# Kernel optimization log

Measured on AMD Instinct MI355X. Metric: run time of the kernel, lower is better.

## Reference

```python
import jax, jax.numpy as jnp
import numpy as np

EPS = 0.05  # blend weight of K_Rectify smoothing


def k_rectify(x_nbc, distance, idx, eps=EPS):
    """Distance-weighted neighbor smoothing.
    x_nbc: (N, B, C); distance, idx: (B, N, K). Returns (N, B, C)."""
    x_bnc = jnp.transpose(x_nbc, (1, 0, 2))                       # (B,N,C)
    B = x_bnc.shape[0]
    neigh = x_bnc[jnp.arange(B)[:, None, None], idx]              # (B,N,K,C) gather
    w = jax.nn.softmax(-distance, axis=-1)                        # closer -> larger weight
    smoothed = jnp.einsum('bnk,bnkc->bnc', w, neigh)              # (B,N,C)
    y = (1.0 - eps) * x_bnc + eps * smoothed
    return jnp.transpose(y, (1, 0, 2))


def monarch_linear(x, w1, w2, bias):
    """Monarch block-diagonal butterfly multiply on the last dim.
    w1: (k,q,p), w2: (l,s,r) with k*p == n, l*r == k*q."""
    shp = x.shape
    k, q, p = w1.shape
    l, s, r = w2.shape
    xb = x.reshape(-1, k, p)
    o1 = jnp.einsum('kqp,bkp->bkq', w1, xb)                       # (B*, k, q)
    o1 = o1.reshape(-1, r, l).transpose(0, 2, 1)                  # 'b (r l) -> b l r'
    o2 = jnp.einsum('lsr,blr->bls', w2, o1)                       # (B*, l, s)
    out = o2.transpose(0, 2, 1).reshape(-1, s * l) + bias         # 'b l s -> b (s l)'
    return out.reshape(*shp[:-1], s * l)


def setup_inputs() -> dict:
    key = jax.random.key(0)
    B, N, C, K, nblocks = 8, 8192, 256, 8, 8
    blk = C // nblocks
    ks = jax.random.split(key, 6)
    x = jax.random.normal(ks[0], (B, N, C), dtype=jnp.float32)
    distance = jax.random.uniform(ks[1], (B, N, K), dtype=jnp.float32)
    idx = jax.random.randint(ks[2], (B, N, K), 0, N)
    rf = jax.random.normal(ks[3], (B, N, C), dtype=jnp.float32)
    scale = 1.0 / np.sqrt(blk)
    w1 = jax.random.normal(ks[4], (nblocks, blk, blk), dtype=jnp.float32) * scale
    w2 = jax.random.normal(ks[5], (nblocks, blk, blk), dtype=jnp.float32) * scale
    bias = jnp.zeros((C,), dtype=jnp.float32)
    return {"x": x, "distance": distance, "idx": idx, "rf": rf,
            "w1": w1, "w2": w2, "bias": bias}


def reference(x, distance, idx, rf, w1, w2, bias):
    # _prepare_in: (B,N,C) -> (N,B,C)
    xs = jnp.transpose(x, (1, 0, 2))
    s1 = k_rectify(xs, distance, idx)            # smooth_in
    t = monarch_linear(s1, w1, w2, bias)         # Monarch block-diag matmul
    s2 = k_rectify(t, distance, idx)             # smooth_out
    return jnp.transpose(s2, (1, 0, 2)) + rf     # _out_transform residual
```

## Files before the change

kernel.cpp:

```cpp
#include <hip/hip_runtime.h>

#define NPTS 8192
#define CH   256
#define KNB  8
#define NROWS 65536
#define ROWS_PER_BLK 16
#define ROWS_PER_IT  4
#define FT_STRIDE 36

typedef unsigned short ushort_t;

__device__ __forceinline__ ushort_t f32_to_bf16(float f) {
    unsigned int b = __float_as_uint(f);
    b += 0x7FFFu + ((b >> 16) & 1u);
    return (ushort_t)(b >> 16);
}
__device__ __forceinline__ float bf16_to_f32(ushort_t u) {
    return __uint_as_float(((unsigned int)u) << 16);
}
__device__ __forceinline__ unsigned int pack_bf16(float lo, float hi) {
    return (unsigned int)f32_to_bf16(lo) | ((unsigned int)f32_to_bf16(hi) << 16);
}

__global__ __launch_bounds__(256) void pm_conv(
    const float4* __restrict__ x, uint4* __restrict__ xb)
{
    const size_t i = (size_t)blockIdx.x * 256 + threadIdx.x;
    const float4 a = x[2 * i];
    const float4 c = x[2 * i + 1];
    uint4 o;
    o.x = pack_bf16(a.x, a.y);
    o.y = pack_bf16(a.z, a.w);
    o.z = pack_bf16(c.x, c.y);
    o.w = pack_bf16(c.z, c.w);
    xb[i] = o;
}

__global__ __launch_bounds__(256) void pm_stage1(
    const ushort_t* __restrict__ xb, const float* __restrict__ dist,
    const int* __restrict__ idx, const float* __restrict__ w1,
    const float* __restrict__ w2, const float* __restrict__ bias,
    ushort_t* __restrict__ t)
{
    const int c = threadIdx.x;

    __shared__ float s1[ROWS_PER_IT][CH];
    __shared__ float fT[ROWS_PER_IT][8 * FT_STRIDE];

    float4 w1r[8], w2r[8];
    {
        const float4* w1p = (const float4*)(w1 + c * 32);
        const float4* w2p = (const float4*)(w2 + ((c & 7) * 32 + (c >> 3)) * 32);
#pragma unroll
        for (int i = 0; i < 8; ++i) { w1r[i] = w1p[i]; w2r[i] = w2p[i]; }
    }
    const float bb = bias[c];
    const int l2   = c & 7;
    const int kb   = c >> 5;
    const int ftw  = l2 * FT_STRIDE + (c >> 3);

    const int rr   = __builtin_amdgcn_readfirstlane(threadIdx.x >> 6);
    const int lane = threadIdx.x & 63;

    const int row_base = blockIdx.x * ROWS_PER_BLK;
    const int b = row_base >> 13;
    const ushort4* x4 = (const ushort4*)(xb + (size_t)b * NPTS * CH);

    for (int it = 0; it < ROWS_PER_BLK / ROWS_PER_IT; ++it) {
        const int row  = row_base + it * ROWS_PER_IT + rr;
        const int rloc = row & (NPTS - 1);

        float d[KNB]; int nb[KNB];
#pragma unroll
        for (int k = 0; k < KNB; ++k) {
            d[k]  = dist[(size_t)row * KNB + k];
            nb[k] = idx[(size_t)row * KNB + k];
        }

        const ushort4 c0 = x4[(size_t)rloc * 64 + lane];
        ushort4 g[KNB];
#pragma unroll
        for (int k = 0; k < KNB; ++k) g[k] = x4[(size_t)nb[k] * 64 + lane];

        float mn = d[0];
#pragma unroll
        for (int k = 1; k < KNB; ++k) mn = fminf(mn, d[k]);
        float e[KNB]; float sum = 0.f;
#pragma unroll
        for (int k = 0; k < KNB; ++k) { e[k] = __expf(mn - d[k]); sum += e[k]; }
        const float inv = 0.05f / sum;

        float4 acc;
        acc.x = 0.95f * bf16_to_f32(c0.x);
        acc.y = 0.95f * bf16_to_f32(c0.y);
        acc.z = 0.95f * bf16_to_f32(c0.z);
        acc.w = 0.95f * bf16_to_f32(c0.w);
#pragma unroll
        for (int k = 0; k < KNB; ++k) {
            const float w = e[k] * inv;
            acc.x += w * bf16_to_f32(g[k].x);
            acc.y += w * bf16_to_f32(g[k].y);
            acc.z += w * bf16_to_f32(g[k].z);
            acc.w += w * bf16_to_f32(g[k].w);
        }
        ((float4*)&s1[rr][0])[lane] = acc;
        __syncthreads();

#pragma unroll
        for (int r2 = 0; r2 < ROWS_PER_IT; ++r2) {
            const float4* sb = (const float4*)(&s1[r2][kb * 32]);
            float a = 0.f;
#pragma unroll
            for (int p4 = 0; p4 < 8; ++p4) {
                const float4 s = sb[p4];
                a += w1r[p4].x * s.x + w1r[p4].y * s.y
                   + w1r[p4].z * s.z + w1r[p4].w * s.w;
            }
            fT[r2][ftw] = a;
        }
        __syncthreads();

#pragma unroll
        for (int r2 = 0; r2 < ROWS_PER_IT; ++r2) {
            const float4* fp = (const float4*)(&fT[r2][l2 * FT_STRIDE]);
            float a = bb;
#pragma unroll
            for (int r4 = 0; r4 < 8; ++r4) {
                const float4 f = fp[r4];
                a += w2r[r4].x * f.x + w2r[r4].y * f.y
                   + w2r[r4].z * f.z + w2r[r4].w * f.w;
            }
            t[(size_t)(row_base + it * ROWS_PER_IT + r2) * CH + c] = f32_to_bf16(a);
        }
        __syncthreads();
    }
}

__global__ __launch_bounds__(256) void pm_stage2(
    const ushort_t* __restrict__ t, const float* __restrict__ dist,
    const int* __restrict__ idx, const float* __restrict__ rf,
    float* __restrict__ out)
{
    const int w     = __builtin_amdgcn_readfirstlane(threadIdx.x >> 6);
    const int lane  = threadIdx.x & 63;
    const int wrow0 = blockIdx.x * 16 + w * 4;
    const int b     = wrow0 >> 13;
    const ushort4* tb = (const ushort4*)(t + (size_t)b * NPTS * CH);

    int   nb[4][KNB];
    float d [4][KNB];
#pragma unroll
    for (int r = 0; r < 4; ++r)
#pragma unroll
        for (int k = 0; k < KNB; ++k) {
            nb[r][k] = idx[(size_t)(wrow0 + r) * KNB + k];
            d [r][k] = dist[(size_t)(wrow0 + r) * KNB + k];
        }

    ushort4 c0[4], g[4][KNB];
    float4  rv[4];
#pragma unroll
    for (int r = 0; r < 4; ++r) {
        const int rloc = (wrow0 + r) & (NPTS - 1);
        c0[r] = tb[(size_t)rloc * 64 + lane];
        rv[r] = ((const float4*)rf)[(size_t)(wrow0 + r) * 64 + lane];
#pragma unroll
        for (int k = 0; k < KNB; ++k) g[r][k] = tb[(size_t)nb[r][k] * 64 + lane];
    }

#pragma unroll
    for (int r = 0; r < 4; ++r) {
        float mn = d[r][0];
#pragma unroll
        for (int k = 1; k < KNB; ++k) mn = fminf(mn, d[r][k]);
        float e[KNB]; float sum = 0.f;
#pragma unroll
        for (int k = 0; k < KNB; ++k) { e[k] = __expf(mn - d[r][k]); sum += e[k]; }
        const float inv = 0.05f / sum;

        float4 acc;
        acc.x = 0.95f * bf16_to_f32(c0[r].x) + rv[r].x;
        acc.y = 0.95f * bf16_to_f32(c0[r].y) + rv[r].y;
        acc.z = 0.95f * bf16_to_f32(c0[r].z) + rv[r].z;
        acc.w = 0.95f * bf16_to_f32(c0[r].w) + rv[r].w;
#pragma unroll
        for (int k = 0; k < KNB; ++k) {
            const float wk = e[k] * inv;
            acc.x += wk * bf16_to_f32(g[r][k].x);
            acc.y += wk * bf16_to_f32(g[r][k].y);
            acc.z += wk * bf16_to_f32(g[r][k].z);
            acc.w += wk * bf16_to_f32(g[r][k].w);
        }
        ((float4*)out)[(size_t)(wrow0 + r) * 64 + lane] = acc;
    }
}

extern "C" void kernel_launch(void* const* d_in, const int* in_sizes, int n_in,
                              void* d_out, int out_size, void* d_ws, size_t ws_size,
                              hipStream_t stream) {
    const float* x    = (const float*)d_in[0];
    const float* dist = (const float*)d_in[1];
    const int*   idx  = (const int*)d_in[2];
    const float* rf   = (const float*)d_in[3];
    const float* w1   = (const float*)d_in[4];
    const float* w2   = (const float*)d_in[5];
    const float* bias = (const float*)d_in[6];
    float* out = (float*)d_out;

    ushort_t* t  = (ushort_t*)d_ws;
    ushort_t* xb = (ushort_t*)((char*)d_ws + (size_t)NROWS * CH * 2);

    pm_conv  <<<NROWS * CH / (256 * 8), 256, 0, stream>>>((const float4*)x, (uint4*)xb);
    pm_stage1<<<NROWS / ROWS_PER_BLK, 256, 0, stream>>>(xb, dist, idx, w1, w2, bias, t);
    pm_stage2<<<NROWS / 16, 256, 0, stream>>>(t, dist, idx, rf, out);
}
```

Baseline: 279.2 us.

## Swizzle blocks across XCDs, use nontemporal streams, double stage1 rows per block

Remaps block indices so that consecutive logical blocks land on the same XCD, keeping each XCD's gathers within a contiguous batch slice of its L2. Streaming loads and stores (x, rf, t, out) are marked nontemporal so they do not evict the gather working set. Stage1 now handles 32 rows per block, spreading the per-block weight-register load over more rows. In exchange there are half as many stage1 blocks, and the nontemporal store of t may lower its cache hit rate when stage2 reads it back.

```diff
diff --git a/kernel.cpp b/kernel.cpp
--- a/kernel.cpp
+++ b/kernel.cpp
@@ -4,11 +4,20 @@
 #define CH   256
 #define KNB  8
 #define NROWS 65536
-#define ROWS_PER_BLK 16
+#define ROWS_PER_BLK 32
 #define ROWS_PER_IT  4
 #define FT_STRIDE 36
 
+#define NBLK_CONV 8192
+#define NBLK_S1   (NROWS / ROWS_PER_BLK)
+#define NBLK_S2   (NROWS / 16)
+
 typedef unsigned short ushort_t;
+typedef float  f32x4  __attribute__((ext_vector_type(4)));
+
+__device__ __forceinline__ int xcd_swz(int h, int cpx) {
+    return (h & 7) * cpx + (h >> 3);
+}
 
 __device__ __forceinline__ ushort_t f32_to_bf16(float f) {
     unsigned int b = __float_as_uint(f);
@@ -23,11 +32,12 @@
 }
 
 __global__ __launch_bounds__(256) void pm_conv(
-    const float4* __restrict__ x, uint4* __restrict__ xb)
+    const f32x4* __restrict__ x, uint4* __restrict__ xb)
 {
-    const size_t i = (size_t)blockIdx.x * 256 + threadIdx.x;
-    const float4 a = x[2 * i];
-    const float4 c = x[2 * i + 1];
+    const int l = xcd_swz(blockIdx.x, NBLK_CONV / 8);
+    const size_t i = (size_t)l * 256 + threadIdx.x;
+    const f32x4 a = __builtin_nontemporal_load(&x[2 * i]);
+    const f32x4 c = __builtin_nontemporal_load(&x[2 * i + 1]);
     uint4 o;
     o.x = pack_bf16(a.x, a.y);
     o.y = pack_bf16(a.z, a.w);
@@ -62,7 +72,8 @@
     const int rr   = __builtin_amdgcn_readfirstlane(threadIdx.x >> 6);
     const int lane = threadIdx.x & 63;
 
-    const int row_base = blockIdx.x * ROWS_PER_BLK;
+    const int lb       = xcd_swz(blockIdx.x, NBLK_S1 / 8);
+    const int row_base = lb * ROWS_PER_BLK;
     const int b = row_base >> 13;
     const ushort4* x4 = (const ushort4*)(xb + (size_t)b * NPTS * CH);
 
@@ -130,7 +141,9 @@
                 a += w2r[r4].x * f.x + w2r[r4].y * f.y
                    + w2r[r4].z * f.z + w2r[r4].w * f.w;
             }
-            t[(size_t)(row_base + it * ROWS_PER_IT + r2) * CH + c] = f32_to_bf16(a);
+            __builtin_nontemporal_store(
+                f32_to_bf16(a),
+                &t[(size_t)(row_base + it * ROWS_PER_IT + r2) * CH + c]);
         }
         __syncthreads();
     }
@@ -143,7 +156,8 @@
 {
     const int w     = __builtin_amdgcn_readfirstlane(threadIdx.x >> 6);
     const int lane  = threadIdx.x & 63;
-    const int wrow0 = blockIdx.x * 16 + w * 4;
+    const int lb    = xcd_swz(blockIdx.x, NBLK_S2 / 8);
+    const int wrow0 = lb * 16 + w * 4;
     const int b     = wrow0 >> 13;
     const ushort4* tb = (const ushort4*)(t + (size_t)b * NPTS * CH);
 
@@ -158,12 +172,13 @@
         }
 
     ushort4 c0[4], g[4][KNB];
-    float4  rv[4];
+    f32x4   rv[4];
 #pragma unroll
     for (int r = 0; r < 4; ++r) {
         const int rloc = (wrow0 + r) & (NPTS - 1);
         c0[r] = tb[(size_t)rloc * 64 + lane];
-        rv[r] = ((const float4*)rf)[(size_t)(wrow0 + r) * 64 + lane];
+        rv[r] = __builtin_nontemporal_load(
+                    &((const f32x4*)rf)[(size_t)(wrow0 + r) * 64 + lane]);
 #pragma unroll
         for (int k = 0; k < KNB; ++k) g[r][k] = tb[(size_t)nb[r][k] * 64 + lane];
     }
@@ -178,7 +193,7 @@
         for (int k = 0; k < KNB; ++k) { e[k] = __expf(mn - d[r][k]); sum += e[k]; }
         const float inv = 0.05f / sum;
 
-        float4 acc;
+        f32x4 acc;
         acc.x = 0.95f * bf16_to_f32(c0[r].x) + rv[r].x;
         acc.y = 0.95f * bf16_to_f32(c0[r].y) + rv[r].y;
         acc.z = 0.95f * bf16_to_f32(c0[r].z) + rv[r].z;
@@ -191,7 +206,8 @@
             acc.z += wk * bf16_to_f32(g[r][k].z);
             acc.w += wk * bf16_to_f32(g[r][k].w);
         }
-        ((float4*)out)[(size_t)(wrow0 + r) * 64 + lane] = acc;
+        __builtin_nontemporal_store(
+            acc, &((f32x4*)out)[(size_t)(wrow0 + r) * 64 + lane]);
     }
 }
 
@@ -210,7 +226,7 @@
     ushort_t* t  = (ushort_t*)d_ws;
     ushort_t* xb = (ushort_t*)((char*)d_ws + (size_t)NROWS * CH * 2);
 
-    pm_conv  <<<NROWS * CH / (256 * 8), 256, 0, stream>>>((const float4*)x, (uint4*)xb);
-    pm_stage1<<<NROWS / ROWS_PER_BLK, 256, 0, stream>>>(xb, dist, idx, w1, w2, bias, t);
-    pm_stage2<<<NROWS / 16, 256, 0, stream>>>(t, dist, idx, rf, out);
-}
+    pm_conv  <<<NBLK_CONV, 256, 0, stream>>>((const f32x4*)x, (uint4*)xb);
+    pm_stage1<<<NBLK_S1,   256, 0, stream>>>(xb, dist, idx, w1, w2, bias, t);
+    pm_stage2<<<NBLK_S2,   256, 0, stream>>>(t, dist, idx, rf, out);
+}
```

After: 270.1 us. 1.03x faster.
